# Kernel optimization log

Measured on AMD Instinct MI355X. Metric: run time of the kernel, lower is better.

## Reference

```python
import jax, jax.numpy as jnp
import numpy as np

VOCAB = 32000
EMBED = 512
HIDDEN = 1024
ATT_L = 64
MAX_LEN = 32
BATCH = 64  # hardcoded in original get_start_states()


def setup_inputs() -> dict:
    key = jax.random.key(0)
    ks = jax.random.split(key, 12)
    s = 0.02
    return {
        "features": jax.random.normal(ks[0], (BATCH, ATT_L, HIDDEN), dtype=jnp.float32),
        "captions": jax.random.randint(ks[1], (BATCH, MAX_LEN), 0, VOCAB),
        "lengths": jnp.full((BATCH,), MAX_LEN - 1, dtype=jnp.int32),  # full lengths (sorted)
        "embed_table": jax.random.normal(ks[2], (VOCAB, EMBED), dtype=jnp.float32) * s,
        "W_ih": jax.random.normal(ks[3], (4 * HIDDEN, EMBED + HIDDEN), dtype=jnp.float32) * s,
        "W_hh": jax.random.normal(ks[4], (4 * HIDDEN, HIDDEN), dtype=jnp.float32) * s,
        "b_ih": jax.random.normal(ks[5], (4 * HIDDEN,), dtype=jnp.float32) * s,
        "b_hh": jax.random.normal(ks[6], (4 * HIDDEN,), dtype=jnp.float32) * s,
        "attn_W": jax.random.normal(ks[7], (ATT_L, EMBED + HIDDEN), dtype=jnp.float32) * s,
        "attn_b": jax.random.normal(ks[8], (ATT_L,), dtype=jnp.float32) * s,
        "lin_W": jax.random.normal(ks[9], (VOCAB, HIDDEN), dtype=jnp.float32) * s,
        "lin_b": jax.random.normal(ks[10], (VOCAB,), dtype=jnp.float32) * s,
    }


def reference(features, captions, lengths, embed_table, W_ih, W_hh, b_ih, b_hh,
              attn_W, attn_b, lin_W, lin_b):
    B = features.shape[0]
    T = captions.shape[1] - 1  # loop runs max_seq_length - 1 steps
    emb = embed_table[captions]              # (B, S, E)
    xs = jnp.transpose(emb[:, :T, :], (1, 0, 2))  # (T, B, E) time-major for scan

    h0 = jnp.zeros((B, HIDDEN), dtype=features.dtype)
    c0 = jnp.zeros((B, HIDDEN), dtype=features.dtype)

    def step(carry, x_t):
        h, c = carry
        # additive-attention branch (softmax over a singleton dim, as in original)
        att_cat = jnp.concatenate([x_t, h], axis=-1) @ attn_W.T + attn_b  # (B, L)
        att_w = jax.nn.softmax(jax.nn.relu(att_cat)[:, None, :], axis=1)  # (B, 1, L) -> all ones
        ctx = jnp.einsum('bol,blh->bh', att_w, features)                  # (B, H)
        # LSTM step (PyTorch gate order: i, f, g, o)
        lstm_in = jnp.concatenate([x_t, ctx], axis=-1)  # (B, E+H)
        gates = lstm_in @ W_ih.T + b_ih + h @ W_hh.T + b_hh
        i, f, g, o = jnp.split(gates, 4, axis=-1)
        c_new = jax.nn.sigmoid(f) * c + jax.nn.sigmoid(i) * jnp.tanh(g)
        h_new = jax.nn.sigmoid(o) * jnp.tanh(c_new)
        return (h_new, c_new), h_new

    _, hs = jax.lax.scan(step, (h0, c0), xs)  # (T, B, H)
    logits = hs @ lin_W.T + lin_b             # (T, B, V)
    # pack_padded_sequence with full lengths == time-major flatten
    return logits.reshape(T * B, -1)
```

## Files before the change

### kernel.cpp

```cpp
#include <hip/hip_runtime.h>
#include <hip/hip_bf16.h>
#include <stdint.h>

#define T_STEPS 31
#define B_ 64
#define E_ 512
#define H_ 1024
#define G4 4096
#define V_ 32000
#define MPAD 2048
#define NREC 64

typedef __bf16 bf16x8_t __attribute__((ext_vector_type(8)));
typedef float f32x4_t __attribute__((ext_vector_type(4)));
typedef unsigned short u16x8_t __attribute__((ext_vector_type(8)));
using bf16 = __hip_bfloat16;

typedef const __attribute__((address_space(1))) unsigned int gas_u32;
typedef __attribute__((address_space(3))) unsigned int las_u32;

__device__ __forceinline__ void async16(const bf16* g, bf16* l) {
    __builtin_amdgcn_global_load_lds((gas_u32*)(uintptr_t)g, (las_u32*)(uintptr_t)l, 16, 0, 0);
}

template<int BM, int BN>
__global__ __launch_bounds__(256)
void gemm_lds(const bf16* __restrict__ A, const bf16* __restrict__ BT,
              float* __restrict__ C, const float* __restrict__ bias,
              int M, int N, int K, int accumulate, int mblocks)
{
    constexpr int BK = 32;
    constexpr int WM = BM / 2, WN = BN / 2;
    constexpr int MI = WM / 16, NI = WN / 16;
    constexpr int AV = (BM * BK) / (8 * 256);
    constexpr int BV = (BN * BK) / (8 * 256);
    static_assert(AV >= 1 && BV >= 1, "tile too small for staging");

    __shared__ bf16 As[BM * BK];
    __shared__ bf16 Bs[BN * BK];

    const int tid = threadIdx.x;
    const int lane = tid & 63;
    const int w = tid >> 6;
    const int wr = w >> 1, wc = w & 1;
    const int quad = lane >> 4, l16 = lane & 15;

    const int nwg = gridDim.x;
    const int bid = blockIdx.x;
    const int q = nwg >> 3, r = nwg & 7;
    const int xcd = bid & 7, o = bid >> 3;
    const int wgid = (xcd < r ? xcd * (q + 1) : r * (q + 1) + (xcd - r) * q) + o;
    const int m0 = (wgid % mblocks) * BM;
    const int n0 = (wgid / mblocks) * BN;

    f32x4_t acc[MI][NI];
#pragma unroll
    for (int i = 0; i < MI; i++)
#pragma unroll
        for (int j = 0; j < NI; j++) acc[i][j] = f32x4_t{0.f, 0.f, 0.f, 0.f};

    for (int kt = 0; kt < K; kt += BK) {
#pragma unroll
        for (int v = 0; v < AV; v++) {
            int idx = tid + v * 256;
            int row = idx >> 2, col = (idx & 3) << 3;
            async16(A + (size_t)(m0 + row) * K + kt + col, As + idx * 8);
        }
#pragma unroll
        for (int v = 0; v < BV; v++) {
            int idx = tid + v * 256;
            int row = idx >> 2, col = (idx & 3) << 3;
            async16(BT + (size_t)(n0 + row) * K + kt + col, Bs + idx * 8);
        }
        __syncthreads();

        bf16x8_t af[MI], bfr[NI];
#pragma unroll
        for (int i = 0; i < MI; i++)
            af[i] = __builtin_bit_cast(bf16x8_t,
                *reinterpret_cast<const u16x8_t*>(&As[(wr * WM + i * 16 + l16) * BK + quad * 8]));
#pragma unroll
        for (int j = 0; j < NI; j++)
            bfr[j] = __builtin_bit_cast(bf16x8_t,
                *reinterpret_cast<const u16x8_t*>(&Bs[(wc * WN + j * 16 + l16) * BK + quad * 8]));
#pragma unroll
        for (int i = 0; i < MI; i++)
#pragma unroll
            for (int j = 0; j < NI; j++)
                acc[i][j] = __builtin_amdgcn_mfma_f32_16x16x32_bf16(af[i], bfr[j], acc[i][j], 0, 0, 0);
        __syncthreads();
    }

#pragma unroll
    for (int i = 0; i < MI; i++) {
        int rbase = m0 + wr * WM + i * 16 + quad * 4;
#pragma unroll
        for (int j = 0; j < NI; j++) {
            int coln = n0 + wc * WN + j * 16 + l16;
            float badd = bias ? bias[coln] : 0.f;
#pragma unroll
            for (int r = 0; r < 4; r++) {
                int grow = rbase + r;
                if (grow < M) {
                    size_t ci = (size_t)grow * N + coln;
                    float val = acc[i][j][r] + badd;
                    if (accumulate) C[ci] += val; else C[ci] = val;
                }
            }
        }
    }
}

__device__ __forceinline__ void grid_barrier(int* bar, int target) {
    __syncthreads();
    if (threadIdx.x == 0) {
        __threadfence();
        atomicAdd(bar, 1);
        while (__hip_atomic_load(bar, __ATOMIC_ACQUIRE, __HIP_MEMORY_SCOPE_AGENT) < target)
            __builtin_amdgcn_s_sleep(2);
        __threadfence();
    }
    __syncthreads();
}

__global__ __launch_bounds__(512)
void recurrence(const bf16* __restrict__ h0, bf16* __restrict__ hs,
                const bf16* __restrict__ Whh, const float* __restrict__ pre_x,
                const float* __restrict__ ctxW, const float* __restrict__ bc,
                int* __restrict__ bar)
{
    __shared__ bf16 Wl[64 * H_];
    __shared__ float gates[64 * 68];

    const int tid = threadIdx.x;
    const int lane = tid & 63;
    const int w = tid >> 6;
    const int wr = w >> 1;
    const int wc = w & 1;
    const int quad = lane >> 4, l16 = lane & 15;
    const int n0 = blockIdx.x * 64;

#pragma unroll 4
    for (int ck = tid; ck < 64 * 128; ck += 512) {
        int row = ck >> 7, c16 = ck & 127;
        u16x8_t v = *reinterpret_cast<const u16x8_t*>(Whh + (size_t)(n0 + row) * H_ + (c16 << 3));
        int byte = (row << 11) + (((c16 << 4)) ^ ((row & 7) << 4));
        *reinterpret_cast<u16x8_t*>(reinterpret_cast<char*>(Wl) + byte) = v;
    }

    const int pb = tid >> 3;
    const int pj = tid & 7;
    const float* cxp = ctxW + (size_t)pb * G4 + n0 + pj * 8;
    const f32x4_t cx0 = *reinterpret_cast<const f32x4_t*>(cxp);
    const f32x4_t cx1 = *reinterpret_cast<const f32x4_t*>(cxp + 4);
    const f32x4_t bc0 = *reinterpret_cast<const f32x4_t*>(bc + n0 + pj * 8);
    const f32x4_t bc1 = *reinterpret_cast<const f32x4_t*>(bc + n0 + pj * 8 + 4);
    float creg0 = 0.f, creg1 = 0.f;

    __syncthreads();

    const int arow = wr * 16 + l16;
    const int r0 = wc * 32 + l16;
    const int xr = (r0 & 7) << 4;
    const char* wl0 = reinterpret_cast<const char*>(Wl) + (r0 << 11);
    const char* wl1 = reinterpret_cast<const char*>(Wl) + ((r0 + 16) << 11);

    int target = NREC;
    for (int t = 0; t < T_STEPS; t++) {
        const float* px = pre_x + ((size_t)t * B_ + pb) * G4 + n0 + pj * 8;
        f32x4_t p0 = *reinterpret_cast<const f32x4_t*>(px);
        f32x4_t p1 = *reinterpret_cast<const f32x4_t*>(px + 4);

        const bf16* hp = t ? hs + (size_t)(t - 1) * B_ * H_ : h0;
        const bf16* ha = hp + (size_t)arow * H_ + quad * 8;

        f32x4_t acc0 = {0.f, 0.f, 0.f, 0.f}, acc1 = {0.f, 0.f, 0.f, 0.f};

#pragma unroll
        for (int kt = 0; kt < H_; kt += 32) {
            int off = ((kt << 1) + (quad << 4)) ^ xr;
            bf16x8_t a  = __builtin_bit_cast(bf16x8_t, *reinterpret_cast<const u16x8_t*>(ha + kt));
            bf16x8_t b0 = __builtin_bit_cast(bf16x8_t, *reinterpret_cast<const u16x8_t*>(wl0 + off));
            bf16x8_t b1 = __builtin_bit_cast(bf16x8_t, *reinterpret_cast<const u16x8_t*>(wl1 + off));
            acc0 = __builtin_amdgcn_mfma_f32_16x16x32_bf16(a, b0, acc0, 0, 0, 0);
            acc1 = __builtin_amdgcn_mfma_f32_16x16x32_bf16(a, b1, acc1, 0, 0, 0);
        }

        {
            int rbase = wr * 16 + quad * 4;
#pragma unroll
            for (int r = 0; r < 4; r++) {
                gates[(rbase + r) * 68 + wc * 32 + l16]      = acc0[r];
                gates[(rbase + r) * 68 + wc * 32 + 16 + l16] = acc1[r];
            }
        }
        __syncthreads();

        {
            f32x4_t g0 = *reinterpret_cast<const f32x4_t*>(&gates[pb * 68 + pj * 8]);
            f32x4_t g1 = *reinterpret_cast<const f32x4_t*>(&gates[pb * 68 + pj * 8 + 4]);
            float gi0 = g0[0] + bc0[0] + p0[0] + cx0[0];
            float gf0 = g0[1] + bc0[1] + p0[1] + cx0[1];
            float gg0 = g0[2] + bc0[2] + p0[2] + cx0[2];
            float go0 = g0[3] + bc0[3] + p0[3] + cx0[3];
            float gi1 = g1[0] + bc1[0] + p1[0] + cx1[0];
            float gf1 = g1[1] + bc1[1] + p1[1] + cx1[1];
            float gg1 = g1[2] + bc1[2] + p1[2] + cx1[2];
            float go1 = g1[3] + bc1[3] + p1[3] + cx1[3];

            float si0 = 1.f / (1.f + expf(-gi0));
            float sf0 = 1.f / (1.f + expf(-gf0));
            float so0 = 1.f / (1.f + expf(-go0));
            float cn0 = sf0 * creg0 + si0 * tanhf(gg0);
            float hn0 = so0 * tanhf(cn0);
            creg0 = cn0;

            float si1 = 1.f / (1.f + expf(-gi1));
            float sf1 = 1.f / (1.f + expf(-gf1));
            float so1 = 1.f / (1.f + expf(-go1));
            float cn1 = sf1 * creg1 + si1 * tanhf(gg1);
            float hn1 = so1 * tanhf(cn1);
            creg1 = cn1;

            int j0 = (n0 >> 2) + pj * 2;
            ushort2 hv;
            hv.x = __builtin_bit_cast(unsigned short, __float2bfloat16(hn0));
            hv.y = __builtin_bit_cast(unsigned short, __float2bfloat16(hn1));
            *reinterpret_cast<ushort2*>(&hs[((size_t)t * B_ + pb) * H_ + j0]) = hv;
        }

        if (t < T_STEPS - 1) {
            grid_barrier(bar, target);
            target += NREC;
        }
    }
}


__global__ __launch_bounds__(256)
void prep_misc(const float* __restrict__ features, const int* __restrict__ captions,
               const float* __restrict__ embed, const float* __restrict__ b_ih,
               const float* __restrict__ b_hh, bf16* __restrict__ ctxcat,
               float* __restrict__ bc, bf16* __restrict__ xs, bf16* __restrict__ h0,
               bf16* __restrict__ hs_tail, int* __restrict__ bar)
{
    const int blk = blockIdx.x, tid = threadIdx.x;
    if (blk < 64) {
        int b = blk;
        for (int j = tid; j < H_; j += 256) {
            float s = 0.f;
            const float* f = features + (size_t)b * 64 * H_ + j;
#pragma unroll
            for (int l = 0; l < 64; l++) s += f[(size_t)l * H_];
            bf16 h = __float2bfloat16(s);
            bf16 lo = __float2bfloat16(s - __bfloat162float(h));
            ctxcat[(size_t)b * 3072 + j] = h;
            ctxcat[(size_t)b * 3072 + 1024 + j] = lo;
            ctxcat[(size_t)b * 3072 + 2048 + j] = h;
        }
    } else if (blk < 80) {
        int g = (blk - 64) * 256 + tid;
        bc[(g & (H_ - 1)) * 4 + (g >> 10)] = b_ih[g] + b_hh[g];
    } else if (blk < 4176) {
        int idx = (blk - 80) * 256 + tid;
        int tb = idx >> 9, e = idx & (E_ - 1);
        float v = 0.f;
        if (tb < T_STEPS * B_) {
            int t = tb >> 6, b = tb & 63;
            v = embed[(size_t)captions[b * 32 + t] * E_ + e];
        }
        xs[idx] = __float2bfloat16(v);
    } else if (blk < 4432) {
        h0[(blk - 4176) * 256 + tid] = __float2bfloat16(0.f);
    } else if (blk < 4688) {
        hs_tail[(blk - 4432) * 256 + tid] = __float2bfloat16(0.f);
    } else if (tid == 0) {
        *bar = 0;
    }
}

__device__ __forceinline__ void cvt4(const float* __restrict__ src, bf16* hi, bf16* hi2, bf16* lo)
{
    f32x4_t v = *reinterpret_cast<const f32x4_t*>(src);
#pragma unroll
    for (int q = 0; q < 4; q++) {
        bf16 h = __float2bfloat16(v[q]);
        hi[q] = h;
        if (hi2) hi2[q] = h;
        if (lo) lo[q] = __float2bfloat16(v[q] - __bfloat162float(h));
    }
}

__global__ __launch_bounds__(256)
void prep_weights(const float* __restrict__ W_ih, const float* __restrict__ W_hh,
                  const float* __restrict__ lin_W, bf16* __restrict__ Wx,
                  bf16* __restrict__ Wc_cat, bf16* __restrict__ Whh, bf16* __restrict__ WlinB)
{
    const int blk = blockIdx.x;
    if (blk < 2048) {
        int item = blk * 256 + threadIdx.x;
        int e = item * 4; int r = e >> 9; int ci = e & (E_ - 1);
        int ro = (r & (H_ - 1)) * 4 + (r >> 10);
        cvt4(W_ih + (size_t)r * (E_ + H_) + ci, Wx + (size_t)ro * E_ + ci, nullptr, nullptr);
    } else if (blk < 6144) {
        int item = (blk - 2048) * 256 + threadIdx.x;
        int e = item * 4; int r = e >> 10; int ci = e & (H_ - 1);
        int ro = (r & (H_ - 1)) * 4 + (r >> 10);
        bf16* base = Wc_cat + (size_t)ro * 3072 + ci;
        cvt4(W_ih + (size_t)r * (E_ + H_) + E_ + ci, base, base + 1024, base + 2048);
    } else if (blk < 10240) {
        int item = (blk - 6144) * 256 + threadIdx.x;
        int e = item * 4; int r = e >> 10; int ci = e & (H_ - 1);
        int ro = (r & (H_ - 1)) * 4 + (r >> 10);
        cvt4(W_hh + (size_t)r * H_ + ci, Whh + (size_t)ro * H_ + ci, nullptr, nullptr);
    } else {
        long item = (long)(blk - 10240) * 256 + threadIdx.x;
        long e = item * 4; int r = (int)(e >> 10); int ci = (int)(e & (H_ - 1));
        cvt4(lin_W + (size_t)r * H_ + ci, WlinB + (size_t)r * H_ + ci, nullptr, nullptr);
    }
}

extern "C" void kernel_launch(void* const* d_in, const int* in_sizes, int n_in,
                              void* d_out, int out_size, void* d_ws, size_t ws_size,
                              hipStream_t stream)
{
    (void)in_sizes; (void)n_in; (void)out_size; (void)ws_size;
    const float* features = (const float*)d_in[0];
    const int*   captions = (const int*)d_in[1];
    const float* embed    = (const float*)d_in[3];
    const float* W_ih     = (const float*)d_in[4];
    const float* W_hh     = (const float*)d_in[5];
    const float* b_ih     = (const float*)d_in[6];
    const float* b_hh     = (const float*)d_in[7];
    const float* lin_W    = (const float*)d_in[10];
    const float* lin_b    = (const float*)d_in[11];
    float* out = (float*)d_out;

    char* wp = (char*)d_ws;
    auto alloc = [&](size_t bytes) -> void* {
        void* p = (void*)wp;
        wp += (bytes + 255) & ~(size_t)255;
        return p;
    };
    bf16*  ctxcat = (bf16*)alloc((size_t)B_ * 3072 * 2);
    float* bc     = (float*)alloc((size_t)G4 * 4);
    bf16*  xs     = (bf16*)alloc((size_t)MPAD * E_ * 2);
    bf16*  Wx     = (bf16*)alloc((size_t)G4 * E_ * 2);
    bf16*  Wc_cat = (bf16*)alloc((size_t)G4 * 3072 * 2);
    bf16*  Whh    = (bf16*)alloc((size_t)G4 * H_ * 2);
    bf16*  WlinB  = (bf16*)alloc((size_t)V_ * H_ * 2);
    float* pre_x  = (float*)alloc((size_t)T_STEPS * B_ * G4 * 4);
    float* ctxW   = (float*)alloc((size_t)B_ * G4 * 4);
    bf16*  h0     = (bf16*)alloc((size_t)B_ * H_ * 2);
    bf16*  hs     = (bf16*)alloc((size_t)MPAD * H_ * 2);
    int*   bar    = (int*)alloc(256);

    prep_misc<<<4689, 256, 0, stream>>>(features, captions, embed, b_ih, b_hh,
                                        ctxcat, bc, xs, h0,
                                        hs + (size_t)T_STEPS * B_ * H_, bar);
    prep_weights<<<42240, 256, 0, stream>>>(W_ih, W_hh, lin_W, Wx, Wc_cat, Whh, WlinB);

    gemm_lds<64, 64><<<G4 / 64, 256, 0, stream>>>(ctxcat, Wc_cat, ctxW, nullptr, B_, G4, 3072, 0, 1);

    gemm_lds<128, 128><<<(MPAD / 128) * (G4 / 128), 256, 0, stream>>>(
        xs, Wx, pre_x, nullptr, T_STEPS * B_, G4, E_, 0, MPAD / 128);

    recurrence<<<NREC, 512, 0, stream>>>(h0, hs, Whh, pre_x, ctxW, bc, bar);

    gemm_lds<128, 128><<<(MPAD / 128) * (V_ / 128), 256, 0, stream>>>(
        hs, WlinB, out, lin_b, T_STEPS * B_, V_, H_, 0, MPAD / 128);
}
```

Baseline: 1.144 ms.

## Merge prep kernels, prefetch recurrence operands, and relax grid barrier ordering

The two preparation kernels become one launch, which saves a launch and lets the small jobs overlap with the weight conversion. In the recurrence kernel, all 32 h-row fragments are loaded into registers before the MFMA loop, and the next step's pre_x values are prefetched while the current step runs. The grid barrier loses its threadfences and acquire load, and hidden states are written with relaxed agent-scope atomic stores, to cut per-step synchronisation latency. Relaxed ordering risks stale h reads across blocks, and the 32-register prefetch raises register pressure under the new two-blocks-per-SM launch bound.

```diff
diff --git a/kernel.cpp b/kernel.cpp
--- a/kernel.cpp
+++ b/kernel.cpp
@@ -111,19 +111,7 @@
     }
 }
 
-__device__ __forceinline__ void grid_barrier(int* bar, int target) {
-    __syncthreads();
-    if (threadIdx.x == 0) {
-        __threadfence();
-        atomicAdd(bar, 1);
-        while (__hip_atomic_load(bar, __ATOMIC_ACQUIRE, __HIP_MEMORY_SCOPE_AGENT) < target)
-            __builtin_amdgcn_s_sleep(2);
-        __threadfence();
-    }
-    __syncthreads();
-}
-
-__global__ __launch_bounds__(512)
+__global__ __launch_bounds__(512, 2)
 void recurrence(const bf16* __restrict__ h0, bf16* __restrict__ hs,
                 const bf16* __restrict__ Whh, const float* __restrict__ pre_x,
                 const float* __restrict__ ctxW, const float* __restrict__ bc,
@@ -157,6 +145,10 @@
     const f32x4_t bc1 = *reinterpret_cast<const f32x4_t*>(bc + n0 + pj * 8 + 4);
     float creg0 = 0.f, creg1 = 0.f;
 
+    const float* px0 = pre_x + (size_t)pb * G4 + n0 + pj * 8;
+    f32x4_t p0 = *reinterpret_cast<const f32x4_t*>(px0);
+    f32x4_t p1 = *reinterpret_cast<const f32x4_t*>(px0 + 4);
+
     __syncthreads();
 
     const int arow = wr * 16 + l16;
@@ -167,19 +159,24 @@
 
     int target = NREC;
     for (int t = 0; t < T_STEPS; t++) {
-        const float* px = pre_x + ((size_t)t * B_ + pb) * G4 + n0 + pj * 8;
-        f32x4_t p0 = *reinterpret_cast<const f32x4_t*>(px);
-        f32x4_t p1 = *reinterpret_cast<const f32x4_t*>(px + 4);
-
         const bf16* hp = t ? hs + (size_t)(t - 1) * B_ * H_ : h0;
         const bf16* ha = hp + (size_t)arow * H_ + quad * 8;
 
+        u16x8_t hr[32];
+#pragma unroll
+        for (int kk = 0; kk < 32; kk++)
+            hr[kk] = *reinterpret_cast<const u16x8_t*>(ha + kk * 32);
+
+        int tn = (t + 1 < T_STEPS) ? t + 1 : t;
+        const float* pxn = pre_x + ((size_t)tn * B_ + pb) * G4 + n0 + pj * 8;
+        f32x4_t p0n = *reinterpret_cast<const f32x4_t*>(pxn);
+        f32x4_t p1n = *reinterpret_cast<const f32x4_t*>(pxn + 4);
+
         f32x4_t acc0 = {0.f, 0.f, 0.f, 0.f}, acc1 = {0.f, 0.f, 0.f, 0.f};
-
-#pragma unroll
-        for (int kt = 0; kt < H_; kt += 32) {
-            int off = ((kt << 1) + (quad << 4)) ^ xr;
-            bf16x8_t a  = __builtin_bit_cast(bf16x8_t, *reinterpret_cast<const u16x8_t*>(ha + kt));
+#pragma unroll
+        for (int kk = 0; kk < 32; kk++) {
+            int off = ((kk << 6) + (quad << 4)) ^ xr;
+            bf16x8_t a  = __builtin_bit_cast(bf16x8_t, hr[kk]);
             bf16x8_t b0 = __builtin_bit_cast(bf16x8_t, *reinterpret_cast<const u16x8_t*>(wl0 + off));
             bf16x8_t b1 = __builtin_bit_cast(bf16x8_t, *reinterpret_cast<const u16x8_t*>(wl1 + off));
             acc0 = __builtin_amdgcn_mfma_f32_16x16x32_bf16(a, b0, acc0, 0, 0, 0);
@@ -223,26 +220,49 @@
             creg1 = cn1;
 
             int j0 = (n0 >> 2) + pj * 2;
-            ushort2 hv;
-            hv.x = __builtin_bit_cast(unsigned short, __float2bfloat16(hn0));
-            hv.y = __builtin_bit_cast(unsigned short, __float2bfloat16(hn1));
-            *reinterpret_cast<ushort2*>(&hs[((size_t)t * B_ + pb) * H_ + j0]) = hv;
-        }
+            uint32_t hv = (uint32_t)__builtin_bit_cast(unsigned short, __float2bfloat16(hn0))
+                        | ((uint32_t)__builtin_bit_cast(unsigned short, __float2bfloat16(hn1)) << 16);
+            __hip_atomic_store(
+                reinterpret_cast<uint32_t*>(&hs[((size_t)t * B_ + pb) * H_ + j0]),
+                hv, __ATOMIC_RELAXED, __HIP_MEMORY_SCOPE_AGENT);
+        }
+
+        p0 = p0n; p1 = p1n;
 
         if (t < T_STEPS - 1) {
-            grid_barrier(bar, target);
+            __syncthreads();
+            if (tid == 0) {
+                __hip_atomic_fetch_add(bar, 1, __ATOMIC_RELAXED, __HIP_MEMORY_SCOPE_AGENT);
+                while (__hip_atomic_load(bar, __ATOMIC_RELAXED, __HIP_MEMORY_SCOPE_AGENT) < target)
+                    __builtin_amdgcn_s_sleep(1);
+            }
+            __syncthreads();
             target += NREC;
         }
     }
 }
 
+__device__ __forceinline__ void cvt4(const float* __restrict__ src, bf16* hi, bf16* hi2, bf16* lo)
+{
+    f32x4_t v = *reinterpret_cast<const f32x4_t*>(src);
+#pragma unroll
+    for (int q = 0; q < 4; q++) {
+        bf16 h = __float2bfloat16(v[q]);
+        hi[q] = h;
+        if (hi2) hi2[q] = h;
+        if (lo) lo[q] = __float2bfloat16(v[q] - __bfloat162float(h));
+    }
+}
 
 __global__ __launch_bounds__(256)
-void prep_misc(const float* __restrict__ features, const int* __restrict__ captions,
-               const float* __restrict__ embed, const float* __restrict__ b_ih,
-               const float* __restrict__ b_hh, bf16* __restrict__ ctxcat,
-               float* __restrict__ bc, bf16* __restrict__ xs, bf16* __restrict__ h0,
-               bf16* __restrict__ hs_tail, int* __restrict__ bar)
+void prep_all(const float* __restrict__ features, const int* __restrict__ captions,
+              const float* __restrict__ embed, const float* __restrict__ b_ih,
+              const float* __restrict__ b_hh, const float* __restrict__ W_ih,
+              const float* __restrict__ W_hh, const float* __restrict__ lin_W,
+              bf16* __restrict__ ctxcat, float* __restrict__ bc, bf16* __restrict__ xs,
+              bf16* __restrict__ Wx, bf16* __restrict__ Wc_cat, bf16* __restrict__ Whh,
+              bf16* __restrict__ WlinB, bf16* __restrict__ h0, bf16* __restrict__ hs_tail,
+              int* __restrict__ bar)
 {
     const int blk = blockIdx.x, tid = threadIdx.x;
     if (blk < 64) {
@@ -258,11 +278,31 @@
             ctxcat[(size_t)b * 3072 + 1024 + j] = lo;
             ctxcat[(size_t)b * 3072 + 2048 + j] = h;
         }
-    } else if (blk < 80) {
-        int g = (blk - 64) * 256 + tid;
-        bc[(g & (H_ - 1)) * 4 + (g >> 10)] = b_ih[g] + b_hh[g];
-    } else if (blk < 4176) {
-        int idx = (blk - 80) * 256 + tid;
+    } else if (blk < 42304) {
+        int wblk = blk - 64;
+        if (wblk < 2048) {
+            int item = wblk * 256 + tid;
+            int e = item * 4; int r = e >> 9; int ci = e & (E_ - 1);
+            int ro = (r & (H_ - 1)) * 4 + (r >> 10);
+            cvt4(W_ih + (size_t)r * (E_ + H_) + ci, Wx + (size_t)ro * E_ + ci, nullptr, nullptr);
+        } else if (wblk < 6144) {
+            int item = (wblk - 2048) * 256 + tid;
+            int e = item * 4; int r = e >> 10; int ci = e & (H_ - 1);
+            int ro = (r & (H_ - 1)) * 4 + (r >> 10);
+            bf16* base = Wc_cat + (size_t)ro * 3072 + ci;
+            cvt4(W_ih + (size_t)r * (E_ + H_) + E_ + ci, base, base + 1024, base + 2048);
+        } else if (wblk < 10240) {
+            int item = (wblk - 6144) * 256 + tid;
+            int e = item * 4; int r = e >> 10; int ci = e & (H_ - 1);
+            int ro = (r & (H_ - 1)) * 4 + (r >> 10);
+            cvt4(W_hh + (size_t)r * H_ + ci, Whh + (size_t)ro * H_ + ci, nullptr, nullptr);
+        } else {
+            long item = (long)(wblk - 10240) * 256 + tid;
+            long e = item * 4; int r = (int)(e >> 10); int ci = (int)(e & (H_ - 1));
+            cvt4(lin_W + (size_t)r * H_ + ci, WlinB + (size_t)r * H_ + ci, nullptr, nullptr);
+        }
+    } else if (blk < 46400) {
+        int idx = (blk - 42304) * 256 + tid;
         int tb = idx >> 9, e = idx & (E_ - 1);
         float v = 0.f;
         if (tb < T_STEPS * B_) {
@@ -270,53 +310,15 @@
             v = embed[(size_t)captions[b * 32 + t] * E_ + e];
         }
         xs[idx] = __float2bfloat16(v);
-    } else if (blk < 4432) {
-        h0[(blk - 4176) * 256 + tid] = __float2bfloat16(0.f);
-    } else if (blk < 4688) {
-        hs_tail[(blk - 4432) * 256 + tid] = __float2bfloat16(0.f);
+    } else if (blk < 46416) {
+        int g = (blk - 46400) * 256 + tid;
+        bc[(g & (H_ - 1)) * 4 + (g >> 10)] = b_ih[g] + b_hh[g];
+    } else if (blk < 46672) {
+        h0[(blk - 46416) * 256 + tid] = __float2bfloat16(0.f);
+    } else if (blk < 46928) {
+        hs_tail[(blk - 46672) * 256 + tid] = __float2bfloat16(0.f);
     } else if (tid == 0) {
         *bar = 0;
-    }
-}
-
-__device__ __forceinline__ void cvt4(const float* __restrict__ src, bf16* hi, bf16* hi2, bf16* lo)
-{
-    f32x4_t v = *reinterpret_cast<const f32x4_t*>(src);
-#pragma unroll
-    for (int q = 0; q < 4; q++) {
-        bf16 h = __float2bfloat16(v[q]);
-        hi[q] = h;
-        if (hi2) hi2[q] = h;
-        if (lo) lo[q] = __float2bfloat16(v[q] - __bfloat162float(h));
-    }
-}
-
-__global__ __launch_bounds__(256)
-void prep_weights(const float* __restrict__ W_ih, const float* __restrict__ W_hh,
-                  const float* __restrict__ lin_W, bf16* __restrict__ Wx,
-                  bf16* __restrict__ Wc_cat, bf16* __restrict__ Whh, bf16* __restrict__ WlinB)
-{
-    const int blk = blockIdx.x;
-    if (blk < 2048) {
-        int item = blk * 256 + threadIdx.x;
-        int e = item * 4; int r = e >> 9; int ci = e & (E_ - 1);
-        int ro = (r & (H_ - 1)) * 4 + (r >> 10);
-        cvt4(W_ih + (size_t)r * (E_ + H_) + ci, Wx + (size_t)ro * E_ + ci, nullptr, nullptr);
-    } else if (blk < 6144) {
-        int item = (blk - 2048) * 256 + threadIdx.x;
-        int e = item * 4; int r = e >> 10; int ci = e & (H_ - 1);
-        int ro = (r & (H_ - 1)) * 4 + (r >> 10);
-        bf16* base = Wc_cat + (size_t)ro * 3072 + ci;
-        cvt4(W_ih + (size_t)r * (E_ + H_) + E_ + ci, base, base + 1024, base + 2048);
-    } else if (blk < 10240) {
-        int item = (blk - 6144) * 256 + threadIdx.x;
-        int e = item * 4; int r = e >> 10; int ci = e & (H_ - 1);
-        int ro = (r & (H_ - 1)) * 4 + (r >> 10);
-        cvt4(W_hh + (size_t)r * H_ + ci, Whh + (size_t)ro * H_ + ci, nullptr, nullptr);
-    } else {
-        long item = (long)(blk - 10240) * 256 + threadIdx.x;
-        long e = item * 4; int r = (int)(e >> 10); int ci = (int)(e & (H_ - 1));
-        cvt4(lin_W + (size_t)r * H_ + ci, WlinB + (size_t)r * H_ + ci, nullptr, nullptr);
     }
 }
 
@@ -355,10 +357,10 @@
     bf16*  hs     = (bf16*)alloc((size_t)MPAD * H_ * 2);
     int*   bar    = (int*)alloc(256);
 
-    prep_misc<<<4689, 256, 0, stream>>>(features, captions, embed, b_ih, b_hh,
-                                        ctxcat, bc, xs, h0,
-                                        hs + (size_t)T_STEPS * B_ * H_, bar);
-    prep_weights<<<42240, 256, 0, stream>>>(W_ih, W_hh, lin_W, Wx, Wc_cat, Whh, WlinB);
+    prep_all<<<46929, 256, 0, stream>>>(features, captions, embed, b_ih, b_hh,
+                                        W_ih, W_hh, lin_W,
+                                        ctxcat, bc, xs, Wx, Wc_cat, Whh, WlinB,
+                                        h0, hs + (size_t)T_STEPS * B_ * H_, bar);
 
     gemm_lds<64, 64><<<G4 / 64, 256, 0, stream>>>(ctxcat, Wc_cat, ctxW, nullptr, B_, G4, 3072, 0, 1);
 
```

New measurement: 1.032 ms. 9.8% less time.
